# Optimization experiments

Hardware: AMD Instinct MI355X
Metric: run time of the kernel (lower is better)

## Reference

```python
import jax, jax.numpy as jnp
import numpy as np

D_MODEL = 1024
N_HEAD = 16
D_K = 64
D_V = 64
LN_EPS = 1e-5


def setup_inputs() -> dict:
    key = jax.random.key(0)
    ks = jax.random.split(key, 12)
    B, S = 4, 2048
    s = 1.0 / np.sqrt(D_MODEL)
    inp = {
        "q": jax.random.normal(ks[0], (B, S, D_MODEL), jnp.float32),
        "k": jax.random.normal(ks[1], (B, S, D_MODEL), jnp.float32),
        "v": jax.random.normal(ks[2], (B, S, D_MODEL), jnp.float32),
        "mask": jnp.ones((B, S, S), jnp.int32),
        "w_q": jax.random.normal(ks[3], (D_MODEL, N_HEAD * D_K), jnp.float32) * s,
        "b_q": jnp.zeros((N_HEAD * D_K,), jnp.float32),
        "w_k": jax.random.normal(ks[4], (D_MODEL, N_HEAD * D_K), jnp.float32) * s,
        "b_k": jnp.zeros((N_HEAD * D_K,), jnp.float32),
        "w_v": jax.random.normal(ks[5], (D_MODEL, N_HEAD * D_V), jnp.float32) * s,
        "b_v": jnp.zeros((N_HEAD * D_V,), jnp.float32),
        "w_fc": jax.random.normal(ks[6], (N_HEAD * D_V, D_MODEL), jnp.float32) * s,
        "b_fc": jnp.zeros((D_MODEL,), jnp.float32),
        "ln_g": jnp.ones((D_MODEL,), jnp.float32),
        "ln_b": jnp.zeros((D_MODEL,), jnp.float32),
    }
    return inp


def reference(q, k, v, mask, w_q, b_q, w_k, b_k, w_v, b_v, w_fc, b_fc, ln_g, ln_b):
    B, Sq, _ = q.shape
    Sk = k.shape[1]
    residual = q
    # QKV projections -> [B, H, S, d]
    qh = (q @ w_q + b_q).reshape(B, Sq, N_HEAD, D_K).transpose(0, 2, 1, 3)
    kh = (k @ w_k + b_k).reshape(B, Sk, N_HEAD, D_K).transpose(0, 2, 1, 3)
    vh = (v @ w_v + b_v).reshape(B, Sk, N_HEAD, D_V).transpose(0, 2, 1, 3)
    temp = jnp.sqrt(jnp.asarray(D_K, qh.dtype))
    scores = jnp.einsum("bhqd,bhkd->bhqk", qh / temp, kh)
    scores = jnp.where(mask[:, None, :, :] == 0, jnp.asarray(-1e9, scores.dtype), scores)
    attn = jax.nn.softmax(scores, axis=-1)  # dropout is identity in eval
    out = jnp.einsum("bhqk,bhkd->bhqd", attn, vh)
    out = out.transpose(0, 2, 1, 3).reshape(B, Sq, N_HEAD * D_V)
    out = out @ w_fc + b_fc  # output proj (dropout identity)
    x = out + residual
    mu = jnp.mean(x, axis=-1, keepdims=True)
    var = jnp.mean(jnp.square(x - mu), axis=-1, keepdims=True)
    y = (x - mu) * jax.lax.rsqrt(var + LN_EPS) * ln_g + ln_b
    return (y, attn)
```

## Files before the change

kernel.cpp:

```cpp
#include <hip/hip_runtime.h>
#include <cstdint>
#include <cstddef>

#define DM 1024
#define HN 16
#define DH 64
#define BB 4
#define SS 2048
#define MM (BB * SS)

typedef __bf16 bf16;
typedef bf16 bf16x8 __attribute__((ext_vector_type(8)));
typedef bf16 bf16x4 __attribute__((ext_vector_type(4)));
typedef float f32x4 __attribute__((ext_vector_type(4)));
typedef int i32x4 __attribute__((ext_vector_type(4)));

__device__ __forceinline__ f32x4 mfma16(bf16x8 a, bf16x8 b, f32x4 c) {
  return __builtin_amdgcn_mfma_f32_16x16x32_bf16(a, b, c, 0, 0, 0);
}

typedef __attribute__((address_space(3))) void lds_void_t;
typedef __attribute__((address_space(1))) void glob_void_t;

__device__ __forceinline__ void gload16(const void* g, void* l) {
  __builtin_amdgcn_global_load_lds((const glob_void_t*)g, (lds_void_t*)l, 16, 0, 0);
}

__global__ __launch_bounds__(256) void mask_bits(const int* __restrict__ mask,
                                                 unsigned long long* __restrict__ mbits) {
  size_t i = (size_t)blockIdx.x * 256 + threadIdx.x;
  int m = mask[i];
  unsigned long long w = __ballot(m != 0);
  if ((threadIdx.x & 63) == 0) mbits[i >> 6] = w;
}

__global__ __launch_bounds__(256) void cvt3(const float* __restrict__ q,
                                            const float* __restrict__ k,
                                            const float* __restrict__ v,
                                            bf16* __restrict__ dst) {
  int which = blockIdx.y;
  const float* in = which == 0 ? q : which == 1 ? k : v;
  bf16* out = dst + (size_t)which * MM * DM;
  int i = (blockIdx.x * 256 + threadIdx.x) * 8;
  f32x4 a = *(const f32x4*)(in + i);
  f32x4 b = *(const f32x4*)(in + i + 4);
  bf16x8 o;
  o[0] = (bf16)a[0]; o[1] = (bf16)a[1]; o[2] = (bf16)a[2]; o[3] = (bf16)a[3];
  o[4] = (bf16)b[0]; o[5] = (bf16)b[1]; o[6] = (bf16)b[2]; o[7] = (bf16)b[3];
  *(bf16x8*)(out + i) = o;
}

__global__ __launch_bounds__(256) void wtrans4(const float* __restrict__ w_q,
                                               const float* __restrict__ w_k,
                                               const float* __restrict__ w_v,
                                               const float* __restrict__ w_fc,
                                               bf16* __restrict__ WT) {
  int p = blockIdx.z;
  const float* W = p == 0 ? w_q : p == 1 ? w_k : p == 2 ? w_v : w_fc;
  bf16* out = WT + (size_t)p * DM * DM;
  __shared__ float t[32][33];
  int n0 = blockIdx.x * 32, k0 = blockIdx.y * 32;
  int tid = threadIdx.x;
  int r = tid >> 3, c = (tid & 7) * 4;
  f32x4 v = *(const f32x4*)&W[(size_t)(k0 + r) * DM + n0 + c];
  t[r][c] = v[0]; t[r][c + 1] = v[1]; t[r][c + 2] = v[2]; t[r][c + 3] = v[3];
  __syncthreads();
  bf16x4 o;
#pragma unroll
  for (int i = 0; i < 4; ++i) o[i] = (bf16)t[c + i][r];
  *(bf16x4*)&out[(size_t)(n0 + r) * DM + k0 + c] = o;
}

__global__ __launch_bounds__(256) void gemm_qkv(const bf16* __restrict__ Abase,
                                                const bf16* __restrict__ Bt,
                                                const float* __restrict__ b_q,
                                                const float* __restrict__ b_k,
                                                const float* __restrict__ b_v,
                                                bf16* __restrict__ qhh,
                                                bf16* __restrict__ khh,
                                                bf16* __restrict__ vhT) {
  constexpr int K = DM;
  __shared__ bf16 Ab[128 * 32];
  __shared__ bf16 Bb[128 * 32];
  int tid = threadIdx.x, wave = tid >> 6, lane = tid & 63;
  int bm = blockIdx.x * 128, bn = blockIdx.y * 128;
  int proj = bn >> 10;
  const bf16* A = Abase + (size_t)proj * MM * DM;
  const float* bias = proj == 0 ? b_q : proj == 1 ? b_k : b_v;
  int wr = (wave >> 1) * 64, wc = (wave & 1) * 64;
  int fr = lane & 15, kg8 = (lane >> 4) * 8;
  f32x4 acc[4][4] = {};
  int arow = tid >> 2, acol = (tid & 3) * 8;
  const bf16* Ag0 = A + (size_t)(bm + arow) * K + acol;
  const bf16* Ag1 = Ag0 + (size_t)64 * K;
  const bf16* Bg0 = Bt + (size_t)(bn + arow) * K + acol;
  const bf16* Bg1 = Bg0 + (size_t)64 * K;
  char* la = (char*)Ab + wave * 1024;
  char* lb = (char*)Bb + wave * 1024;
  for (int k0 = 0; k0 < K; k0 += 32) {
    __syncthreads();
    gload16(Ag0 + k0, la);
    gload16(Ag1 + k0, la + 4096);
    gload16(Bg0 + k0, lb);
    gload16(Bg1 + k0, lb + 4096);
    asm volatile("s_waitcnt vmcnt(0)" ::: "memory");
    __syncthreads();
    bf16x8 af[4], bfr[4];
#pragma unroll
    for (int m = 0; m < 4; ++m)
      af[m] = *(const bf16x8*)&Ab[(wr + m * 16 + fr) * 32 + kg8];
#pragma unroll
    for (int n = 0; n < 4; ++n)
      bfr[n] = *(const bf16x8*)&Bb[(wc + n * 16 + fr) * 32 + kg8];
#pragma unroll
    for (int m = 0; m < 4; ++m)
#pragma unroll
      for (int n = 0; n < 4; ++n) acc[m][n] = mfma16(af[m], bfr[n], acc[m][n]);
  }
  int b = bm >> 11;
#pragma unroll
  for (int m = 0; m < 4; ++m)
#pragma unroll
    for (int n = 0; n < 4; ++n) {
      int c = bn + wc + n * 16 + fr;
      int lc = c & 1023;
      float bv = bias[lc];
      int h = lc >> 6, d = lc & 63;
      int r0 = bm + wr + m * 16 + (lane >> 4) * 4;
      int s0 = r0 & (SS - 1);
      if (proj == 2) {
        bf16x4 o;
#pragma unroll
        for (int j = 0; j < 4; ++j) o[j] = (bf16)(acc[m][n][j] + bv);
        *(bf16x4*)&vhT[((size_t)(b * HN + h) * DH + d) * SS + s0] = o;
      } else {
        bf16* dst = proj == 0 ? qhh : khh;
        float sc = proj == 0 ? 0.125f : 1.f;
#pragma unroll
        for (int j = 0; j < 4; ++j) {
          float v = (acc[m][n][j] + bv) * sc;
          dst[(size_t)(b * HN + h) * (SS * DH) + (size_t)(s0 + j) * DH + d] =
              (bf16)v;
        }
      }
    }
}

__global__ __launch_bounds__(256) void gemm_out(const bf16* __restrict__ A,
                                                const bf16* __restrict__ Bt,
                                                const float* __restrict__ bias,
                                                const float* __restrict__ resid,
                                                float* __restrict__ out) {
  constexpr int K = DM;
  __shared__ bf16 Ab[128 * 32];
  __shared__ bf16 Bb[128 * 32];
  int tid = threadIdx.x, wave = tid >> 6, lane = tid & 63;
  int bm = blockIdx.x * 128, bn = blockIdx.y * 128;
  int wr = (wave >> 1) * 64, wc = (wave & 1) * 64;
  int fr = lane & 15, kg8 = (lane >> 4) * 8;
  f32x4 acc[4][4] = {};
  int arow = tid >> 2, acol = (tid & 3) * 8;
  const bf16* Ag0 = A + (size_t)(bm + arow) * K + acol;
  const bf16* Ag1 = Ag0 + (size_t)64 * K;
  const bf16* Bg0 = Bt + (size_t)(bn + arow) * K + acol;
  const bf16* Bg1 = Bg0 + (size_t)64 * K;
  char* la = (char*)Ab + wave * 1024;
  char* lb = (char*)Bb + wave * 1024;
  for (int k0 = 0; k0 < K; k0 += 32) {
    __syncthreads();
    gload16(Ag0 + k0, la);
    gload16(Ag1 + k0, la + 4096);
    gload16(Bg0 + k0, lb);
    gload16(Bg1 + k0, lb + 4096);
    asm volatile("s_waitcnt vmcnt(0)" ::: "memory");
    __syncthreads();
    bf16x8 af[4], bfr[4];
#pragma unroll
    for (int m = 0; m < 4; ++m)
      af[m] = *(const bf16x8*)&Ab[(wr + m * 16 + fr) * 32 + kg8];
#pragma unroll
    for (int n = 0; n < 4; ++n)
      bfr[n] = *(const bf16x8*)&Bb[(wc + n * 16 + fr) * 32 + kg8];
#pragma unroll
    for (int m = 0; m < 4; ++m)
#pragma unroll
      for (int n = 0; n < 4; ++n) acc[m][n] = mfma16(af[m], bfr[n], acc[m][n]);
  }
#pragma unroll
  for (int m = 0; m < 4; ++m)
#pragma unroll
    for (int n = 0; n < 4; ++n) {
      int c = bn + wc + n * 16 + fr;
      float bv = bias[c];
#pragma unroll
      for (int j = 0; j < 4; ++j) {
        int r = bm + wr + m * 16 + (lane >> 4) * 4 + j;
        size_t idx = (size_t)r * DM + c;
        out[idx] = acc[m][n][j] + bv + resid[idx];
      }
    }
}

__global__ __launch_bounds__(512, 4) void attn_kernel(
    const bf16* __restrict__ qh, const bf16* __restrict__ kh,
    const bf16* __restrict__ vhT, const unsigned int* __restrict__ mbits,
    float* __restrict__ attn_out, bf16* __restrict__ ctx) {
  extern __shared__ char smem[];
  float* pbuf = (float*)(smem + 16 * 4096);
  float* invp = (float*)(smem + 16 * 4096 + 4096);
  int tid = threadIdx.x, wave = tid >> 6, lane = tid & 63;
  int qt = blockIdx.x, bh = blockIdx.y;
  int b = bh >> 4, h = bh & 15;
  int q0 = qt * 16;
  const bf16* qbase = qh + ((size_t)bh * SS + q0) * DH;
  const bf16* kbase = kh + (size_t)bh * SS * DH;
  const bf16* vbase = vhT + (size_t)bh * SS * DH;
  int fr = lane & 15, kg = lane >> 4;

  bf16x8 qf0 = *(const bf16x8*)&qbase[(size_t)fr * DH + kg * 8];
  bf16x8 qf1 = *(const bf16x8*)&qbase[(size_t)fr * DH + 32 + kg * 8];

  {
    int sw = wave * 256;
    bf16x8 kb0[4], kb1[4];
    auto kload = [&](int g) {
      const bf16* kp = kbase + (size_t)(sw + g * 16 + fr) * DH + kg * 8;
      kb0[g & 3] = *(const bf16x8*)kp;
      kb1[g & 3] = *(const bf16x8*)(kp + 32);
    };
    kload(0);
    kload(1);
    kload(2);
#pragma unroll
    for (int g = 0; g < 16; ++g) {
      if (g < 13) kload(g + 3);
      f32x4 acc = {0.f, 0.f, 0.f, 0.f};
      acc = mfma16(qf0, kb0[g & 3], acc);
      acc = mfma16(qf1, kb1[g & 3], acc);
      int col = sw + g * 16 + fr;
      int slot = col >> 3, within = col & 7;
#pragma unroll
      for (int j = 0; j < 4; ++j) {
        int row = kg * 4 + j;
        *(bf16*)(smem + row * 4096 + ((slot ^ row) << 4) + within * 2) =
            (bf16)acc[j];
      }
    }
  }
  __syncthreads();

  {
    int row = wave * 2 + (lane >> 5);
    int la = lane & 31;
    char* rbase = smem + row * 4096;
    const unsigned int* mrow32 = mbits + ((size_t)b * SS + q0 + row) * 64;
    float sum = 0.f;
#pragma unroll
    for (int it = 0; it < 8; ++it) {
      int slot = la + it * 32;
      char* p = rbase + ((slot ^ row) << 4);
      bf16x8 e = *(const bf16x8*)p;
      unsigned int bits = mrow32[slot >> 2] >> ((slot & 3) * 8);
      bf16x8 w8;
#pragma unroll
      for (int i = 0; i < 8; ++i) {
        float f = __expf((float)e[i]);
        f = ((bits >> i) & 1u) ? f : 0.f;
        sum += f;
        w8[i] = (bf16)f;
      }
      *(bf16x8*)p = w8;
    }
#pragma unroll
    for (int off = 1; off < 32; off <<= 1) sum += __shfl_xor(sum, off);
    float inv = 1.f / sum;
    if (la == 0) invp[row] = inv;
    float* arow_ = attn_out + ((size_t)bh * SS + q0 + row) * SS;
#pragma unroll
    for (int it = 0; it < 8; ++it) {
      int slot = la + it * 32;
      bf16x8 e = *(const bf16x8*)(rbase + ((slot ^ row) << 4));
      f32x4 u0, u1;
#pragma unroll
      for (int i = 0; i < 4; ++i) {
        u0[i] = (float)e[i] * inv;
        u1[i] = (float)e[i + 4] * inv;
      }
      __builtin_nontemporal_store(u0, (f32x4*)&arow_[slot * 8]);
      __builtin_nontemporal_store(u1, (f32x4*)&arow_[slot * 8 + 4]);
    }
  }
  __syncthreads();

  {
    int dq = wave & 3, khalf = wave >> 2;
    f32x4 cacc = {0.f, 0.f, 0.f, 0.f};
    const bf16* vrow = vbase + (size_t)(dq * 16 + fr) * SS + khalf * 1024;
    char* prow = smem + fr * 4096;
    bf16x8 vb[4], pb[4];
    auto pvload = [&](int kk) {
      vb[kk & 3] = *(const bf16x8*)&vrow[kk * 32 + kg * 8];
      int slotA = khalf * 128 + kk * 4 + kg;
      pb[kk & 3] = *(const bf16x8*)(prow + ((slotA ^ fr) << 4));
    };
    pvload(0);
    pvload(1);
    pvload(2);
#pragma unroll
    for (int kk = 0; kk < 32; ++kk) {
      if (kk < 29) pvload(kk + 3);
      cacc = mfma16(pb[kk & 3], vb[kk & 3], cacc);
    }
    if (khalf == 1) {
#pragma unroll
      for (int j = 0; j < 4; ++j)
        pbuf[dq * 256 + (kg * 4 + j) * 16 + fr] = cacc[j];
    }
    __syncthreads();
    if (khalf == 0) {
#pragma unroll
      for (int j = 0; j < 4; ++j) {
        int row = kg * 4 + j;
        float v = (cacc[j] + pbuf[dq * 256 + row * 16 + fr]) * invp[row];
        ctx[((size_t)b * SS + q0 + row) * DM + h * DH + dq * 16 + fr] = (bf16)v;
      }
    }
  }
}

__global__ __launch_bounds__(256) void ln_k(float* __restrict__ x,
                                            const float* __restrict__ g,
                                            const float* __restrict__ bln) {
  int r = blockIdx.x, tid = threadIdx.x;
  f32x4 v = *(const f32x4*)&x[(size_t)r * DM + tid * 4];
  float s = v[0] + v[1] + v[2] + v[3];
  float s2 = v[0] * v[0] + v[1] * v[1] + v[2] * v[2] + v[3] * v[3];
#pragma unroll
  for (int off = 32; off; off >>= 1) {
    s += __shfl_down(s, off);
    s2 += __shfl_down(s2, off);
  }
  __shared__ float rs_[4], rs2_[4];
  int wave = tid >> 6, lane = tid & 63;
  if (lane == 0) {
    rs_[wave] = s;
    rs2_[wave] = s2;
  }
  __syncthreads();
  s = rs_[0] + rs_[1] + rs_[2] + rs_[3];
  s2 = rs2_[0] + rs2_[1] + rs2_[2] + rs2_[3];
  float mu = s * (1.f / DM);
  float var = s2 * (1.f / DM) - mu * mu;
  float rstd = rsqrtf(var + 1e-5f);
  f32x4 gg = *(const f32x4*)&g[tid * 4];
  f32x4 bb = *(const f32x4*)&bln[tid * 4];
  f32x4 o;
#pragma unroll
  for (int i = 0; i < 4; ++i) o[i] = (v[i] - mu) * rstd * gg[i] + bb[i];
  *(f32x4*)&x[(size_t)r * DM + tid * 4] = o;
}

extern "C" void kernel_launch(void* const* d_in, const int* in_sizes, int n_in,
                              void* d_out, int out_size, void* d_ws,
                              size_t ws_size, hipStream_t stream) {
  const float* q = (const float*)d_in[0];
  const float* k = (const float*)d_in[1];
  const float* v = (const float*)d_in[2];
  const int* mask = (const int*)d_in[3];
  const float* w_q = (const float*)d_in[4];
  const float* b_q = (const float*)d_in[5];
  const float* w_k = (const float*)d_in[6];
  const float* b_k = (const float*)d_in[7];
  const float* w_v = (const float*)d_in[8];
  const float* b_v = (const float*)d_in[9];
  const float* w_fc = (const float*)d_in[10];
  const float* b_fc = (const float*)d_in[11];
  const float* ln_g = (const float*)d_in[12];
  const float* ln_b = (const float*)d_in[13];

  float* y = (float*)d_out;
  float* attn_out = (float*)d_out + (size_t)MM * DM;

  char* w = (char*)d_ws;
  const size_t actN = (size_t)MM * DM;
  bf16* qkv_bf = (bf16*)w;  w += 3 * actN * 2;
  bf16* wT = (bf16*)w;      w += (size_t)4 * DM * DM * 2;
  bf16* qhh = (bf16*)w;     w += actN * 2;
  bf16* khh = (bf16*)w;     w += actN * 2;
  bf16* vhT = (bf16*)w;     w += actN * 2;
  bf16* ctx = (bf16*)w;     w += actN * 2;
  unsigned long long* mb = (unsigned long long*)w;  w += (size_t)BB * SS * SS / 8;

  mask_bits<<<(BB * SS * SS) / 256, 256, 0, stream>>>(mask, mb);
  cvt3<<<dim3(4096, 3), 256, 0, stream>>>(q, k, v, qkv_bf);
  wtrans4<<<dim3(DM / 32, DM / 32, 4), 256, 0, stream>>>(w_q, w_k, w_v, w_fc, wT);
  gemm_qkv<<<dim3(MM / 128, 3072 / 128), 256, 0, stream>>>(
      qkv_bf, wT, b_q, b_k, b_v, qhh, khh, vhT);
  hipFuncSetAttribute((const void*)attn_kernel,
                      hipFuncAttributeMaxDynamicSharedMemorySize, 69696);
  attn_kernel<<<dim3(SS / 16, BB * HN), 512, 69696, stream>>>(
      qhh, khh, vhT, (const unsigned int*)mb, attn_out, ctx);
  gemm_out<<<dim3(MM / 128, DM / 128), 256, 0, stream>>>(
      ctx, wT + (size_t)3 * DM * DM, b_fc, q, y);
  ln_k<<<MM, 256, 0, stream>>>(y, ln_g, ln_b);
}
```

Measured before the change: 756.1 us.

## Split attention into context kernel and separate probability-writing recompute kernel

The attention kernel is split in two. The first computes softmax normalizers and the context output without writing the full fp32 attention matrix. A second kernel recomputes QK^T and exp, then streams the normalized probabilities to the output. The aim is to keep the large probability store from stalling the PV phase, at the cost of recomputing the scores and launching an extra kernel. K and V prefetch depths are also increased, which uses more registers.

```diff
diff --git a/kernel.cpp b/kernel.cpp
--- a/kernel.cpp
+++ b/kernel.cpp
@@ -13,7 +13,6 @@
 typedef bf16 bf16x8 __attribute__((ext_vector_type(8)));
 typedef bf16 bf16x4 __attribute__((ext_vector_type(4)));
 typedef float f32x4 __attribute__((ext_vector_type(4)));
-typedef int i32x4 __attribute__((ext_vector_type(4)));
 
 __device__ __forceinline__ f32x4 mfma16(bf16x8 a, bf16x8 b, f32x4 c) {
   return __builtin_amdgcn_mfma_f32_16x16x32_bf16(a, b, c, 0, 0, 0);
@@ -201,10 +200,10 @@
     }
 }
 
-__global__ __launch_bounds__(512, 4) void attn_kernel(
+__global__ __launch_bounds__(512, 4) void attn_core(
     const bf16* __restrict__ qh, const bf16* __restrict__ kh,
     const bf16* __restrict__ vhT, const unsigned int* __restrict__ mbits,
-    float* __restrict__ attn_out, bf16* __restrict__ ctx) {
+    float* __restrict__ invg, bf16* __restrict__ ctx) {
   extern __shared__ char smem[];
   float* pbuf = (float*)(smem + 16 * 4096);
   float* invp = (float*)(smem + 16 * 4096 + 4096);
@@ -222,21 +221,20 @@
 
   {
     int sw = wave * 256;
-    bf16x8 kb0[4], kb1[4];
+    bf16x8 kb0[8], kb1[8];
     auto kload = [&](int g) {
       const bf16* kp = kbase + (size_t)(sw + g * 16 + fr) * DH + kg * 8;
-      kb0[g & 3] = *(const bf16x8*)kp;
-      kb1[g & 3] = *(const bf16x8*)(kp + 32);
+      kb0[g & 7] = *(const bf16x8*)kp;
+      kb1[g & 7] = *(const bf16x8*)(kp + 32);
     };
-    kload(0);
-    kload(1);
-    kload(2);
+#pragma unroll
+    for (int g = 0; g < 6; ++g) kload(g);
 #pragma unroll
     for (int g = 0; g < 16; ++g) {
-      if (g < 13) kload(g + 3);
+      if (g < 10) kload(g + 6);
       f32x4 acc = {0.f, 0.f, 0.f, 0.f};
-      acc = mfma16(qf0, kb0[g & 3], acc);
-      acc = mfma16(qf1, kb1[g & 3], acc);
+      acc = mfma16(qf0, kb0[g & 7], acc);
+      acc = mfma16(qf1, kb1[g & 7], acc);
       int col = sw + g * 16 + fr;
       int slot = col >> 3, within = col & 7;
 #pragma unroll
@@ -274,20 +272,9 @@
 #pragma unroll
     for (int off = 1; off < 32; off <<= 1) sum += __shfl_xor(sum, off);
     float inv = 1.f / sum;
-    if (la == 0) invp[row] = inv;
-    float* arow_ = attn_out + ((size_t)bh * SS + q0 + row) * SS;
-#pragma unroll
-    for (int it = 0; it < 8; ++it) {
-      int slot = la + it * 32;
-      bf16x8 e = *(const bf16x8*)(rbase + ((slot ^ row) << 4));
-      f32x4 u0, u1;
-#pragma unroll
-      for (int i = 0; i < 4; ++i) {
-        u0[i] = (float)e[i] * inv;
-        u1[i] = (float)e[i + 4] * inv;
-      }
-      __builtin_nontemporal_store(u0, (f32x4*)&arow_[slot * 8]);
-      __builtin_nontemporal_store(u1, (f32x4*)&arow_[slot * 8 + 4]);
+    if (la == 0) {
+      invp[row] = inv;
+      invg[(size_t)bh * SS + q0 + row] = inv;
     }
   }
   __syncthreads();
@@ -297,19 +284,20 @@
     f32x4 cacc = {0.f, 0.f, 0.f, 0.f};
     const bf16* vrow = vbase + (size_t)(dq * 16 + fr) * SS + khalf * 1024;
     char* prow = smem + fr * 4096;
-    bf16x8 vb[4], pb[4];
+    bf16x8 vb[8], pb[8];
     auto pvload = [&](int kk) {
-      vb[kk & 3] = *(const bf16x8*)&vrow[kk * 32 + kg * 8];
+      vb[kk & 7] = *(const bf16x8*)&vrow[kk * 32 + kg * 8];
       int slotA = khalf * 128 + kk * 4 + kg;
-      pb[kk & 3] = *(const bf16x8*)(prow + ((slotA ^ fr) << 4));
+      pb[kk & 7] = *(const bf16x8*)(prow + ((slotA ^ fr) << 4));
     };
     pvload(0);
     pvload(1);
     pvload(2);
+    pvload(3);
 #pragma unroll
     for (int kk = 0; kk < 32; ++kk) {
-      if (kk < 29) pvload(kk + 3);
-      cacc = mfma16(pb[kk & 3], vb[kk & 3], cacc);
+      if (kk < 28) pvload(kk + 4);
+      cacc = mfma16(pb[kk & 7], vb[kk & 7], cacc);
     }
     if (khalf == 1) {
 #pragma unroll
@@ -324,6 +312,79 @@
         float v = (cacc[j] + pbuf[dq * 256 + row * 16 + fr]) * invp[row];
         ctx[((size_t)b * SS + q0 + row) * DM + h * DH + dq * 16 + fr] = (bf16)v;
       }
+    }
+  }
+}
+
+__global__ __launch_bounds__(512, 4) void prob_write(
+    const bf16* __restrict__ qh, const bf16* __restrict__ kh,
+    const unsigned int* __restrict__ mbits, const float* __restrict__ invg,
+    float* __restrict__ attn_out) {
+  extern __shared__ char smem[];
+  int tid = threadIdx.x, wave = tid >> 6, lane = tid & 63;
+  int qt = blockIdx.x, bh = blockIdx.y;
+  int b = bh >> 4;
+  int q0 = qt * 16;
+  const bf16* qbase = qh + ((size_t)bh * SS + q0) * DH;
+  const bf16* kbase = kh + (size_t)bh * SS * DH;
+  int fr = lane & 15, kg = lane >> 4;
+
+  bf16x8 qf0 = *(const bf16x8*)&qbase[(size_t)fr * DH + kg * 8];
+  bf16x8 qf1 = *(const bf16x8*)&qbase[(size_t)fr * DH + 32 + kg * 8];
+
+  {
+    int sw = wave * 256;
+    bf16x8 kb0[8], kb1[8];
+    auto kload = [&](int g) {
+      const bf16* kp = kbase + (size_t)(sw + g * 16 + fr) * DH + kg * 8;
+      kb0[g & 7] = *(const bf16x8*)kp;
+      kb1[g & 7] = *(const bf16x8*)(kp + 32);
+    };
+#pragma unroll
+    for (int g = 0; g < 6; ++g) kload(g);
+#pragma unroll
+    for (int g = 0; g < 16; ++g) {
+      if (g < 10) kload(g + 6);
+      f32x4 acc = {0.f, 0.f, 0.f, 0.f};
+      acc = mfma16(qf0, kb0[g & 7], acc);
+      acc = mfma16(qf1, kb1[g & 7], acc);
+      int col = sw + g * 16 + fr;
+      int slot = col >> 3, within = col & 7;
+#pragma unroll
+      for (int j = 0; j < 4; ++j) {
+        int row = kg * 4 + j;
+        *(bf16*)(smem + row * 4096 + ((slot ^ row) << 4) + within * 2) =
+            (bf16)acc[j];
+      }
+    }
+  }
+  __syncthreads();
+
+  {
+    int row = wave * 2 + (lane >> 5);
+    int la = lane & 31;
+    char* rbase = smem + row * 4096;
+    const unsigned int* mrow32 = mbits + ((size_t)b * SS + q0 + row) * 64;
+    float inv = invg[(size_t)bh * SS + q0 + row];
+    float* arow_ = attn_out + ((size_t)bh * SS + q0 + row) * SS;
+#pragma unroll
+    for (int it = 0; it < 8; ++it) {
+      int slot = la + it * 32;
+      bf16x8 e = *(const bf16x8*)(rbase + ((slot ^ row) << 4));
+      unsigned int bits = mrow32[slot >> 2] >> ((slot & 3) * 8);
+      f32x4 u0, u1;
+#pragma unroll
+      for (int i = 0; i < 4; ++i) {
+        float f = __expf((float)e[i]) * inv;
+        u0[i] = ((bits >> i) & 1u) ? f : 0.f;
+      }
+#pragma unroll
+      for (int i = 0; i < 4; ++i) {
+        float f = __expf((float)e[i + 4]) * inv;
+        u1[i] = ((bits >> (i + 4)) & 1u) ? f : 0.f;
+      }
+      __builtin_nontemporal_store(u0, (f32x4*)&arow_[slot * 8]);
+      __builtin_nontemporal_store(u1, (f32x4*)&arow_[slot * 8 + 4]);
     }
   }
 }
@@ -390,16 +451,21 @@
   bf16* vhT = (bf16*)w;     w += actN * 2;
   bf16* ctx = (bf16*)w;     w += actN * 2;
   unsigned long long* mb = (unsigned long long*)w;  w += (size_t)BB * SS * SS / 8;
+  float* invg = (float*)w;  w += (size_t)BB * HN * SS * 4;
 
   mask_bits<<<(BB * SS * SS) / 256, 256, 0, stream>>>(mask, mb);
   cvt3<<<dim3(4096, 3), 256, 0, stream>>>(q, k, v, qkv_bf);
   wtrans4<<<dim3(DM / 32, DM / 32, 4), 256, 0, stream>>>(w_q, w_k, w_v, w_fc, wT);
   gemm_qkv<<<dim3(MM / 128, 3072 / 128), 256, 0, stream>>>(
       qkv_bf, wT, b_q, b_k, b_v, qhh, khh, vhT);
-  hipFuncSetAttribute((const void*)attn_kernel,
+  hipFuncSetAttribute((const void*)attn_core,
                       hipFuncAttributeMaxDynamicSharedMemorySize, 69696);
-  attn_kernel<<<dim3(SS / 16, BB * HN), 512, 69696, stream>>>(
-      qhh, khh, vhT, (const unsigned int*)mb, attn_out, ctx);
+  attn_core<<<dim3(SS / 16, BB * HN), 512, 69696, stream>>>(
+      qhh, khh, vhT, (const unsigned int*)mb, invg, ctx);
+  hipFuncSetAttribute((const void*)prob_write,
+                      hipFuncAttributeMaxDynamicSharedMemorySize, 65536);
+  prob_write<<<dim3(SS / 16, BB * HN), 512, 65536, stream>>>(
+      qhh, khh, (const unsigned int*)mb, invg, attn_out);
   gemm_out<<<dim3(MM / 128, DM / 128), 256, 0, stream>>>(
       ctx, wT + (size_t)3 * DM * DM, b_fc, q, y);
   ln_k<<<MM, 256, 0, stream>>>(y, ln_g, ln_b);
```

Result: slower. 991.3 us (+31.1%).
